# Kernel optimization log

Hardware: AMD Instinct MI355X
Metric: run time of the kernel (lower is better)

## Reference

```python
import jax, jax.numpy as jnp
import numpy as np

H = 2        # attention heads (GENsConv heads=2)
DH = 128     # per-head dim (= hidden_channels; concat=False -> heads averaged)
L = 4        # num message-passing layers actually used (convs[:-1])
NG = 500     # number of graphs in the batch
N = 50000    # total nodes
E = 200000   # total edges
HID = 128    # hidden_channels
RES = 0.1    # initial_res
EPS = 1e-5   # BatchNorm eps (eval mode: running_mean=0, running_var=1)


def _bn(x, g, b):
    # BatchNorm1d in eval mode with default running stats
    return x * (g / jnp.sqrt(1.0 + EPS)) + b


def setup_inputs() -> dict:
    key = jax.random.key(0)
    ks = jax.random.split(key, 32)
    s = 0.05
    d = {}
    d["x"] = jax.random.randint(ks[0], (N,), 0, 30)
    d["edge_index"] = jax.random.randint(ks[1], (2, E), 0, N)
    d["edge_attr"] = jax.random.randint(ks[2], (E,), 0, 30)
    d["batch"] = jnp.sort(jax.random.randint(ks[3], (N,), 0, NG))
    d["node_emb"] = jax.random.normal(ks[4], (30, HID)) * s
    d["emb_w1"] = jax.random.normal(ks[5], (HID, HID)) * s
    d["emb_b1"] = jnp.zeros((HID,))
    d["emb_g1"] = jnp.ones((HID,))
    d["emb_bt1"] = jnp.zeros((HID,))
    d["emb_w2"] = jax.random.normal(ks[6], (HID, HID)) * s
    d["emb_b2"] = jnp.zeros((HID,))
    d["bn0_g"] = jnp.ones((HID,))
    d["bn0_b"] = jnp.zeros((HID,))
    d["Wq"] = jax.random.normal(ks[7], (L, HID, H * DH)) * s
    d["Wk"] = jax.random.normal(ks[8], (L, HID, H * DH)) * s
    d["Wv"] = jax.random.normal(ks[9], (L, HID, H * DH)) * s
    d["We"] = jax.random.normal(ks[10], (L, HID, H * DH)) * s
    d["att"] = jax.random.normal(ks[11], (L, H, DH)) * s
    d["Wroot"] = jax.random.normal(ks[12], (L, HID, HID)) * s
    d["bias"] = jnp.zeros((L, HID))
    d["out_w1"] = jax.random.normal(ks[13], (HID * (L + 1), HID)) * s
    d["out_b1"] = jnp.zeros((HID,))
    d["out_g1"] = jnp.ones((HID,))
    d["out_bt1"] = jnp.zeros((HID,))
    d["out_w2"] = jax.random.normal(ks[14], (HID, 1)) * s
    d["out_b2"] = jnp.zeros((1,))
    return d


def _forward(params, x, edge_index, edge_attr, batch):
    (node_emb, emb_w1, emb_b1, emb_g1, emb_bt1, emb_w2, emb_b2, bn0_g, bn0_b,
     Wq, Wk, Wv, We, att, Wroot, bias,
     out_w1, out_b1, out_g1, out_bt1, out_w2, out_b2) = params
    src, dst = edge_index[0], edge_index[1]
    h = node_emb[x]                      # [N, HID]
    ea = node_emb[edge_attr]             # [E, HID] (original embeds edge_attr with node_embedding)
    # emb_convs: Linear -> BN -> ReLU -> Linear, then bns[0] + ReLU
    h = jax.nn.relu(_bn(h @ emb_w1 + emb_b1, emb_g1, emb_bt1))
    h = h @ emb_w2 + emb_b2
    h = jax.nn.relu(_bn(h, bn0_g, bn0_b))
    x0 = h
    xs = [h]
    for i in range(L):
        hi = xs[-1]
        # gather -> per-edge multi-head attention message -> scatter (GENsConv stand-in)
        q = (hi @ Wq[i]).reshape(N, H, DH)[dst]          # [E, H, DH]
        k = (hi @ Wk[i]).reshape(N, H, DH)[src]
        v = (hi @ Wv[i]).reshape(N, H, DH)[src]
        e = (ea @ We[i]).reshape(E, H, DH)
        score = jnp.einsum('ehd,hd->eh', jax.nn.leaky_relu(q + k + e, 0.2), att[i])
        smax = jax.ops.segment_max(score, dst, num_segments=N)[dst]
        exps = jnp.exp(score - smax)
        denom = jax.ops.segment_sum(exps, dst, num_segments=N)[dst]
        alpha = exps / denom                              # segment softmax over incoming edges
        msg = alpha[..., None] * (v + e)                  # [E, H, DH]
        agg = jax.ops.segment_sum(msg, dst, num_segments=N)  # [N, H, DH]
        out = agg.mean(axis=1) + hi @ Wroot[i] + bias[i]  # concat=False -> average heads, + root
        out = jax.nn.relu(out)
        out = (1.0 - RES) * out + RES * x0                # initial residual
        xs.append(out)
    hc = jnp.concatenate(xs, axis=-1)                     # cat=True -> [N, HID*(L+1)]
    sums = jax.ops.segment_sum(hc, batch, num_segments=NG)
    cnt = jax.ops.segment_sum(jnp.ones((N, 1), hc.dtype), batch, num_segments=NG)
    g = sums / jnp.maximum(cnt, 1.0)                      # global mean pool
    g = jax.nn.relu(_bn(g @ out_w1 + out_b1, out_g1, out_bt1))
    g = g @ out_w2 + out_b2
    return g.reshape(-1)                                  # [NG]


def reference(x, edge_index, edge_attr, batch, node_emb, emb_w1, emb_b1, emb_g1, emb_bt1, emb_w2, emb_b2, bn0_g, bn0_b, Wq, Wk, Wv, We, att, Wroot, bias, out_w1, out_b1, out_g1, out_bt1, out_w2, out_b2):
    params = (node_emb, emb_w1, emb_b1, emb_g1, emb_bt1, emb_w2, emb_b2, bn0_g, bn0_b,
              Wq, Wk, Wv, We, att, Wroot, bias,
              out_w1, out_b1, out_g1, out_bt1, out_w2, out_b2)
    return _forward(params, x, edge_index, edge_attr, batch)
```

## Files before the change

### kernel.cpp

```cpp
#include <hip/hip_runtime.h>
#include <hip/hip_bf16.h>

#define NN 50000
#define NE 200000
#define NGR 500
#define HD 128
#define CDIM 256
#define NLAY 4
#define NVOC 30
#define NCAT 896
#define SCH 256
#define SNB ((NN + SCH - 1) / SCH)
#define GP 7
#define CBP (56 / GP)

static constexpr float BN_INV = 0.9999950000374997f;

typedef __attribute__((ext_vector_type(8))) short bf16x8;
typedef __attribute__((ext_vector_type(4))) float f32x4;
typedef __attribute__((ext_vector_type(2))) float f32x2;

__device__ __forceinline__ float bf2f(unsigned short u) {
    return __uint_as_float(((unsigned)u) << 16);
}
__device__ __forceinline__ unsigned short f2bf(float f) {
    union { __hip_bfloat16 h; unsigned short u; } cv;
    cv.h = __float2bfloat16(f);
    return cv.u;
}
__device__ __forceinline__ f32x2 up2(unsigned u) {
    f32x2 r;
    r.x = __uint_as_float(u << 16);
    r.y = __uint_as_float(u & 0xffff0000u);
    return r;
}
__device__ __forceinline__ f32x2 lk2(f32x2 z) {
    f32x2 zero = {0.f, 0.f};
    return __builtin_elementwise_max(z, zero) + 0.2f * __builtin_elementwise_min(z, zero);
}

__global__ __launch_bounds__(128) void k_tables_node(
    const float* __restrict__ ne, const float* __restrict__ w1, const float* __restrict__ b1,
    const float* __restrict__ g1, const float* __restrict__ bt1,
    const float* __restrict__ w2, const float* __restrict__ b2,
    const float* __restrict__ g0, const float* __restrict__ bt0,
    float* __restrict__ x0tab)
{
    int r = blockIdx.x, d = threadIdx.x;
    __shared__ float emb[HD], t1[HD];
    emb[d] = ne[r * HD + d];
    __syncthreads();
    float acc = b1[d];
    for (int k = 0; k < HD; ++k) acc += emb[k] * w1[k * HD + d];
    float t = fmaxf(acc * BN_INV * g1[d] + bt1[d], 0.f);
    t1[d] = t;
    __syncthreads();
    float acc2 = b2[d];
    for (int k = 0; k < HD; ++k) acc2 += t1[k] * w2[k * HD + d];
    x0tab[r * HD + d] = fmaxf(acc2 * BN_INV * g0[d] + bt0[d], 0.f);
}

__global__ __launch_bounds__(256) void k_tables_edge(
    const float* __restrict__ ne, const float* __restrict__ We, unsigned short* __restrict__ etab)
{
    int la = blockIdx.x;
    int l = la / NVOC, a = la % NVOC;
    int c = threadIdx.x;
    __shared__ float emb[HD];
    if (c < HD) emb[c] = ne[a * HD + c];
    __syncthreads();
    const float* W = We + (size_t)l * HD * CDIM;
    float acc = 0.f;
    for (int k = 0; k < HD; ++k) acc += emb[k] * W[k * CDIM + c];
    etab[(size_t)la * CDIM + c] = f2bf(acc);
}

__global__ __launch_bounds__(64) void k_packw(
    const float* __restrict__ Wq, const float* __restrict__ Wk,
    const float* __restrict__ Wv, const float* __restrict__ Wr,
    unsigned short* __restrict__ Wpk)
{
    int b = blockIdx.x;
    int l = b / 224, rem = b % 224;
    int kb = rem / 56, jb = rem % 56;
    int lane = threadIdx.x;
    int j = jb * 16 + (lane & 15);
    int kbase = kb * 32 + ((lane >> 4) << 3);
    unsigned short* dst = Wpk + ((size_t)b * 64 + lane) * 8;
#pragma unroll
    for (int t = 0; t < 8; ++t) {
        int k = kbase + t;
        float v;
        if (j < 256) {
            v = Wq[((size_t)l * HD + k) * CDIM + j];
        } else if (j < 768) {
            int tt = j - 256, g = tt >> 3, r = tt & 7;
            int c = g * 4 + (r & 3);
            v = (r < 4) ? Wk[((size_t)l * HD + k) * CDIM + c]
                        : Wv[((size_t)l * HD + k) * CDIM + c];
        } else {
            v = Wr[((size_t)l * HD + k) * HD + (j - 768)];
        }
        dst[t] = f2bf(v);
    }
}

__global__ void k_hist_dst(const int* __restrict__ ei, int* __restrict__ cnt)
{
    int e = blockIdx.x * blockDim.x + threadIdx.x;
    if (e < NE) atomicAdd(&cnt[ei[NE + e]], 1);
}

__global__ __launch_bounds__(256) void k_blocksum(const int* __restrict__ cnt, int* __restrict__ part)
{
    int t = threadIdx.x;
    int i = blockIdx.x * SCH + t;
    int v = (i < NN) ? cnt[i] : 0;
    __shared__ int sm[256];
    sm[t] = v;
    __syncthreads();
    for (int off = 128; off; off >>= 1) {
        if (t < off) sm[t] += sm[t + off];
        __syncthreads();
    }
    if (t == 0) part[blockIdx.x] = sm[0];
}

__global__ __launch_bounds__(256) void k_scanpart(int* __restrict__ part)
{
    int t = threadIdx.x;
    int v = (t < SNB) ? part[t] : 0;
    __shared__ int sm[256];
    sm[t] = v;
    __syncthreads();
    for (int off = 1; off < 256; off <<= 1) {
        int u = (t >= off) ? sm[t - off] : 0;
        __syncthreads();
        sm[t] += u;
        __syncthreads();
    }
    if (t < SNB) part[t] = sm[t] - v;
}

__global__ __launch_bounds__(256) void k_csrwrite(
    const int* __restrict__ cnt, const int* __restrict__ part,
    int* __restrict__ rowp, int* __restrict__ wof)
{
    int t = threadIdx.x;
    int i = blockIdx.x * SCH + t;
    int v = (i < NN) ? cnt[i] : 0;
    __shared__ int sm[256];
    sm[t] = v;
    __syncthreads();
    for (int off = 1; off < 256; off <<= 1) {
        int u = (t >= off) ? sm[t - off] : 0;
        __syncthreads();
        sm[t] += u;
        __syncthreads();
    }
    int excl = sm[t] - v + part[blockIdx.x];
    if (i < NN) { rowp[i] = excl; wof[i] = excl; }
    if (i == NN - 1) rowp[NN] = excl + v;
}

__global__ void k_scatter(const int* __restrict__ ei, const int* __restrict__ ea,
                          int* __restrict__ wof, int2* __restrict__ cse)
{
    int e = blockIdx.x * blockDim.x + threadIdx.x;
    if (e < NE) {
        int d = ei[NE + e];
        int pos = atomicAdd(&wof[d], 1);
        int2 v; v.x = ei[e]; v.y = ea[e];
        cse[pos] = v;
    }
}

__global__ void k_x0(const int* __restrict__ x, const float* __restrict__ tab,
                     unsigned short* __restrict__ x0b,
                     const int* __restrict__ batch, int* __restrict__ gptr)
{
    int idx = blockIdx.x * blockDim.x + threadIdx.x;
    if (idx <= NGR) {
        if (idx == NGR) gptr[idx] = NN;
        else {
            int lo = 0, hi = NN;
            while (lo < hi) { int mid = (lo + hi) >> 1; if (batch[mid] < idx) lo = mid + 1; else hi = mid; }
            gptr[idx] = lo;
        }
    }
    if (idx >= NN * 32) return;
    int n = idx >> 5, c = idx & 31;
    float4 v = *(const float4*)&tab[x[n] * HD + c * 4];
    ushort4 u; u.x = f2bf(v.x); u.y = f2bf(v.y); u.z = f2bf(v.z); u.w = f2bf(v.w);
    *(ushort4*)&x0b[(size_t)n * HD + c * 4] = u;
}

__global__ __launch_bounds__(256) void k_gemm(
    const unsigned short* __restrict__ Ab, const unsigned short* __restrict__ Wpk,
    unsigned short* __restrict__ C)
{
    __shared__ unsigned short tile[64][136];
    int lane = threadIdx.x & 63, wid = threadIdx.x >> 6;
    int nb = blockIdx.x * 64;
    int rowl = wid * 16 + (lane & 15);
    int node = nb + rowl;
    size_t arow = (size_t)((node < NN) ? node : (NN - 1));
    int ko = (lane >> 4) << 3;
    const unsigned short* ap = Ab + arow * HD + ko;
    bf16x8 a0 = *(const bf16x8*)(ap);
    bf16x8 a1 = *(const bf16x8*)(ap + 32);
    bf16x8 a2 = *(const bf16x8*)(ap + 64);
    bf16x8 a3 = *(const bf16x8*)(ap + 96);

    int cb0 = blockIdx.y * CBP;
    const unsigned short* bp = Wpk + (size_t)cb0 * 512 + (size_t)lane * 8;
    int jreg = (lane >> 4) << 2;
#pragma unroll 4
    for (int i = 0; i < CBP; ++i) {
        bf16x8 w0 = *(const bf16x8*)(bp + i * 512);
        bf16x8 w1 = *(const bf16x8*)(bp + i * 512 + 28672);
        bf16x8 w2 = *(const bf16x8*)(bp + i * 512 + 57344);
        bf16x8 w3 = *(const bf16x8*)(bp + i * 512 + 86016);
        f32x4 acc = {0.f, 0.f, 0.f, 0.f};
        acc = __builtin_amdgcn_mfma_f32_16x16x32_bf16(w0, a0, acc, 0, 0, 0);
        acc = __builtin_amdgcn_mfma_f32_16x16x32_bf16(w1, a1, acc, 0, 0, 0);
        acc = __builtin_amdgcn_mfma_f32_16x16x32_bf16(w2, a2, acc, 0, 0, 0);
        acc = __builtin_amdgcn_mfma_f32_16x16x32_bf16(w3, a3, acc, 0, 0, 0);
        uint2 o;
        o.x = (unsigned)f2bf(acc[0]) | ((unsigned)f2bf(acc[1]) << 16);
        o.y = (unsigned)f2bf(acc[2]) | ((unsigned)f2bf(acc[3]) << 16);
        *(uint2*)&tile[rowl][i * 16 + jreg] = o;
    }
    __syncthreads();
    int r0 = threadIdx.x >> 4;
    int cseg = (threadIdx.x & 15) * 8;
#pragma unroll
    for (int pass = 0; pass < 4; ++pass) {
        int row = pass * 16 + r0;
        int gnode = nb + row;
        if (gnode < NN) {
            uint4 v = *(const uint4*)&tile[row][cseg];
            *(uint4*)&C[(size_t)gnode * NCAT + cb0 * 16 + cseg] = v;
        }
    }
}

__global__ __launch_bounds__(256) void k_edge(
    const unsigned short* __restrict__ QKVR,
    const unsigned short* __restrict__ etab,
    const float* __restrict__ attL, const float* __restrict__ biasL,
    const unsigned short* __restrict__ x0b,
    const int* __restrict__ rowptr, const int2* __restrict__ cse,
    unsigned short* __restrict__ hb)
{
    int n = (blockIdx.x * blockDim.x + threadIdx.x) >> 6;
    if (n >= NN) return;
    int lane = threadIdx.x & 63;
    int head = lane >> 5, sub = lane & 31;
    int col = head * HD + sub * 4;
    int kvo = 256 + head * 256 + sub * 8;

    uint2 quu = *(const uint2*)&QKVR[(size_t)n * NCAT + col];
    f32x2 q0 = up2(quu.x), q1 = up2(quu.y);
    float4 a4 = *(const float4*)&attL[col];
    f32x2 av0 = {a4.x, a4.y}, av1 = {a4.z, a4.w};

    float l0 = 0.f, l1 = 0.f;
    f32x2 accA0 = {0.f, 0.f}, accA1 = {0.f, 0.f};
    f32x2 accB0 = {0.f, 0.f}, accB1 = {0.f, 0.f};

    int beg = rowptr[n], end = rowptr[n + 1];
    int idx = beg;
    for (; idx + 1 < end; idx += 2) {
        int2 seA = cse[idx];
        int2 seB = cse[idx + 1];
        uint4 kvA = *(const uint4*)&QKVR[(size_t)seA.x * NCAT + kvo];
        uint4 kvB = *(const uint4*)&QKVR[(size_t)seB.x * NCAT + kvo];
        uint2 euA = *(const uint2*)&etab[seA.y * CDIM + col];
        uint2 euB = *(const uint2*)&etab[seB.y * CDIM + col];

        f32x2 eA0 = up2(euA.x), eA1 = up2(euA.y);
        f32x2 eB0 = up2(euB.x), eB1 = up2(euB.y);

        f32x2 zA0 = lk2(q0 + up2(kvA.x) + eA0);
        f32x2 zA1 = lk2(q1 + up2(kvA.y) + eA1);
        f32x2 zB0 = lk2(q0 + up2(kvB.x) + eB0);
        f32x2 zB1 = lk2(q1 + up2(kvB.y) + eB1);

        f32x2 ppA = zA0 * av0 + zA1 * av1;
        f32x2 ppB = zB0 * av0 + zB1 * av1;
        float pA = ppA.x + ppA.y;
        float pB = ppB.x + ppB.y;
        pA += __shfl_xor(pA, 16); pB += __shfl_xor(pB, 16);
        pA += __shfl_xor(pA, 8);  pB += __shfl_xor(pB, 8);
        pA += __shfl_xor(pA, 4);  pB += __shfl_xor(pB, 4);
        pA += __shfl_xor(pA, 2);  pB += __shfl_xor(pB, 2);
        pA += __shfl_xor(pA, 1);  pB += __shfl_xor(pB, 1);
        float peA = __expf(fminf(fmaxf(pA, -30.f), 30.f));
        float peB = __expf(fminf(fmaxf(pB, -30.f), 30.f));

        accA0 += peA * (up2(kvA.z) + eA0);
        accA1 += peA * (up2(kvA.w) + eA1);
        accB0 += peB * (up2(kvB.z) + eB0);
        accB1 += peB * (up2(kvB.w) + eB1);
        l0 += peA;
        l1 += peB;
    }
    if (idx < end) {
        int2 se = cse[idx];
        uint4 kv = *(const uint4*)&QKVR[(size_t)se.x * NCAT + kvo];
        uint2 eu = *(const uint2*)&etab[se.y * CDIM + col];
        f32x2 e0 = up2(eu.x), e1 = up2(eu.y);
        f32x2 z0 = lk2(q0 + up2(kv.x) + e0);
        f32x2 z1 = lk2(q1 + up2(kv.y) + e1);
        f32x2 pp = z0 * av0 + z1 * av1;
        float p = pp.x + pp.y;
        p += __shfl_xor(p, 16); p += __shfl_xor(p, 8);
        p += __shfl_xor(p, 4);  p += __shfl_xor(p, 2); p += __shfl_xor(p, 1);
        float pe = __expf(fminf(fmaxf(p, -30.f), 30.f));
        accA0 += pe * (up2(kv.z) + e0);
        accA1 += pe * (up2(kv.w) + e1);
        l0 += pe;
    }
    float l = l0 + l1;
    float invl = (l > 0.f) ? 1.0f / l : 0.f;
    f32x2 r0 = (accA0 + accB0) * invl;
    f32x2 r1 = (accA1 + accB1) * invl;
    r0.x = 0.5f * (r0.x + __shfl_xor(r0.x, 32));
    r0.y = 0.5f * (r0.y + __shfl_xor(r0.y, 32));
    r1.x = 0.5f * (r1.x + __shfl_xor(r1.x, 32));
    r1.y = 0.5f * (r1.y + __shfl_xor(r1.y, 32));
    if (head == 0) {
        uint2 ruu = *(const uint2*)&QKVR[(size_t)n * NCAT + 768 + sub * 4];
        f32x2 ru0 = up2(ruu.x), ru1 = up2(ruu.y);
        float4 b4 = *(const float4*)&biasL[sub * 4];
        f32x2 bb0 = {b4.x, b4.y}, bb1 = {b4.z, b4.w};
        uint2 xuu = *(const uint2*)&x0b[(size_t)n * HD + sub * 4];
        f32x2 xx0 = up2(xuu.x), xx1 = up2(xuu.y);
        f32x2 zero = {0.f, 0.f};
        f32x2 h0 = 0.9f * __builtin_elementwise_max(r0 + ru0 + bb0, zero) + 0.1f * xx0;
        f32x2 h1 = 0.9f * __builtin_elementwise_max(r1 + ru1 + bb1, zero) + 0.1f * xx1;
        ushort4 o;
        o.x = f2bf(h0.x); o.y = f2bf(h0.y); o.z = f2bf(h1.x); o.w = f2bf(h1.y);
        *(ushort4*)&hb[(size_t)n * HD + sub * 4] = o;
    }
}

__global__ __launch_bounds__(256) void k_poolall(
    const unsigned short* __restrict__ x0b,
    const unsigned short* __restrict__ h0, const unsigned short* __restrict__ h1,
    const unsigned short* __restrict__ h2, const unsigned short* __restrict__ h3,
    const int* __restrict__ gptr, float* __restrict__ gsum)
{
    int g = blockIdx.x, sl = blockIdx.y;
    const unsigned short* src = (sl == 0) ? x0b : (sl == 1) ? h0 : (sl == 2) ? h1
                              : (sl == 3) ? h2 : h3;
    int q = threadIdx.x & 31;
    int r = threadIdx.x >> 5;
    int beg = gptr[g], end = gptr[g + 1];
    float sx = 0.f, sy = 0.f, sz = 0.f, sw = 0.f;
    for (int n = beg + r; n < end; n += 8) {
        uint2 u = *(const uint2*)&src[(size_t)n * HD + q * 4];
        sx += __uint_as_float(u.x << 16);
        sy += __uint_as_float(u.x & 0xffff0000u);
        sz += __uint_as_float(u.y << 16);
        sw += __uint_as_float(u.y & 0xffff0000u);
    }
    __shared__ float4 sm[8][32];
    float4 s4 = {sx, sy, sz, sw};
    sm[r][q] = s4;
    __syncthreads();
    if (r == 0) {
        float4 t = sm[0][q];
#pragma unroll
        for (int j = 1; j < 8; ++j) {
            float4 u = sm[j][q];
            t.x += u.x; t.y += u.y; t.z += u.z; t.w += u.w;
        }
        *(float4*)&gsum[(size_t)g * 640 + sl * HD + q * 4] = t;
    }
}

__global__ __launch_bounds__(128) void k_out(
    const float* __restrict__ gsum, const int* __restrict__ gptr,
    const float* __restrict__ w1, const float* __restrict__ b1,
    const float* __restrict__ g1, const float* __restrict__ bt1,
    const float* __restrict__ w2, const float* __restrict__ b2,
    float* __restrict__ out)
{
    int g = blockIdx.x, d = threadIdx.x;
    __shared__ float row[640];
    __shared__ float red[2];
    int c = gptr[g + 1] - gptr[g];
    float invc = 1.0f / (float)max(c, 1);
    for (int j = d; j < 640; j += 128) row[j] = gsum[(size_t)g * 640 + j] * invc;
    __syncthreads();
    float acc = b1[d];
    for (int j = 0; j < 640; ++j) acc += row[j] * w1[j * HD + d];
    float val = fmaxf(acc * BN_INV * g1[d] + bt1[d], 0.f);
    float part = val * w2[d];
    part += __shfl_xor(part, 32); part += __shfl_xor(part, 16);
    part += __shfl_xor(part, 8);  part += __shfl_xor(part, 4);
    part += __shfl_xor(part, 2);  part += __shfl_xor(part, 1);
    if ((threadIdx.x & 63) == 0) red[threadIdx.x >> 6] = part;
    __syncthreads();
    if (threadIdx.x == 0) out[g] = red[0] + red[1] + b2[0];
}

extern "C" void kernel_launch(void* const* d_in, const int* in_sizes, int n_in,
                              void* d_out, int out_size, void* d_ws, size_t ws_size,
                              hipStream_t stream)
{
    const int*   x        = (const int*)d_in[0];
    const int*   ei       = (const int*)d_in[1];
    const int*   ea       = (const int*)d_in[2];
    const int*   batch    = (const int*)d_in[3];
    const float* node_emb = (const float*)d_in[4];
    const float* emb_w1   = (const float*)d_in[5];
    const float* emb_b1   = (const float*)d_in[6];
    const float* emb_g1   = (const float*)d_in[7];
    const float* emb_bt1  = (const float*)d_in[8];
    const float* emb_w2   = (const float*)d_in[9];
    const float* emb_b2   = (const float*)d_in[10];
    const float* bn0_g    = (const float*)d_in[11];
    const float* bn0_b    = (const float*)d_in[12];
    const float* Wq       = (const float*)d_in[13];
    const float* Wk       = (const float*)d_in[14];
    const float* Wv       = (const float*)d_in[15];
    const float* We       = (const float*)d_in[16];
    const float* att      = (const float*)d_in[17];
    const float* Wroot    = (const float*)d_in[18];
    const float* bias     = (const float*)d_in[19];
    const float* out_w1   = (const float*)d_in[20];
    const float* out_b1   = (const float*)d_in[21];
    const float* out_g1   = (const float*)d_in[22];
    const float* out_bt1  = (const float*)d_in[23];
    const float* out_w2   = (const float*)d_in[24];
    const float* out_b2   = (const float*)d_in[25];

    char* wp = (char*)d_ws;
    auto alloc = [&](size_t bytes) -> void* {
        void* p = (void*)wp;
        wp += (bytes + 255) & ~(size_t)255;
        return p;
    };
    unsigned short* x0b   = (unsigned short*)alloc((size_t)NN * HD * 2);
    unsigned short* hb0   = (unsigned short*)alloc((size_t)NN * HD * 2);
    unsigned short* hb1   = (unsigned short*)alloc((size_t)NN * HD * 2);
    unsigned short* hb2   = (unsigned short*)alloc((size_t)NN * HD * 2);
    unsigned short* hb3   = (unsigned short*)alloc((size_t)NN * HD * 2);
    unsigned short* QKVR  = (unsigned short*)alloc((size_t)NN * NCAT * 2);
    float*          x0tab = (float*)alloc((size_t)NVOC * HD * 4);
    unsigned short* etab  = (unsigned short*)alloc((size_t)NLAY * NVOC * CDIM * 2);
    unsigned short* Wpk   = (unsigned short*)alloc((size_t)NLAY * 224 * 64 * 8 * 2);
    int*   cnt   = (int*)alloc((size_t)NN * 4);
    int*   rowp  = (int*)alloc((size_t)(NN + 1) * 4);
    int*   wof   = (int*)alloc((size_t)(NN + 1) * 4);
    int*   part  = (int*)alloc((size_t)SNB * 4);
    int2*  cse   = (int2*)alloc((size_t)NE * 8);
    int*   gptr  = (int*)alloc((size_t)(NGR + 1) * 4);
    float* gsum  = (float*)alloc((size_t)NGR * 640 * 4);

    hipMemsetAsync(cnt, 0, (size_t)NN * 4, stream);

    k_tables_node<<<NVOC, 128, 0, stream>>>(node_emb, emb_w1, emb_b1, emb_g1, emb_bt1,
                                            emb_w2, emb_b2, bn0_g, bn0_b, x0tab);
    k_tables_edge<<<NLAY * NVOC, 256, 0, stream>>>(node_emb, We, etab);
    k_packw<<<NLAY * 224, 64, 0, stream>>>(Wq, Wk, Wv, Wroot, Wpk);
    k_hist_dst<<<(NE + 255) / 256, 256, 0, stream>>>(ei, cnt);
    k_blocksum<<<SNB, 256, 0, stream>>>(cnt, part);
    k_scanpart<<<1, 256, 0, stream>>>(part);
    k_csrwrite<<<SNB, 256, 0, stream>>>(cnt, part, rowp, wof);
    k_scatter<<<(NE + 255) / 256, 256, 0, stream>>>(ei, ea, wof, cse);
    k_x0<<<(NN * 32 + 255) / 256, 256, 0, stream>>>(x, x0tab, x0b, batch, gptr);

    const unsigned short* hin = x0b;
    unsigned short* houts[NLAY] = {hb0, hb1, hb2, hb3};
    for (int l = 0; l < NLAY; ++l) {
        k_gemm<<<dim3((NN + 63) / 64, GP), 256, 0, stream>>>(
            hin, Wpk + (size_t)l * 224 * 512, QKVR);
        k_edge<<<(NN * 64 + 255) / 256, 256, 0, stream>>>(
            QKVR, etab + (size_t)l * NVOC * CDIM, att + (size_t)l * CDIM, bias + (size_t)l * HD,
            x0b, rowp, cse, houts[l]);
        hin = houts[l];
    }
    k_poolall<<<dim3(NGR, 5), 256, 0, stream>>>(x0b, hb0, hb1, hb2, hb3, gptr, gsum);
    k_out<<<NGR, 128, 0, stream>>>(gsum, gptr, out_w1, out_b1, out_g1, out_bt1,
                                   out_w2, out_b2, (float*)d_out);
}
```

Measured before the change: 409.3 us.

## Merge setup kernels into one launch and software-pipeline edge gathers

Four independent setup kernels (node table, edge table, weight packing, destination histogram) are combined into a single launch that dispatches on block index, removing three launch gaps. Separately, the edge aggregation loop now prefetches the next pair of neighbor K/V and edge-table rows before computing on the current pair, to hide gather latency. The prefetch raises register pressure in the edge kernel, which may lower occupancy.

```diff
diff --git a/kernel.cpp b/kernel.cpp
--- a/kernel.cpp
+++ b/kernel.cpp
@@ -14,6 +14,12 @@
 #define GP 7
 #define CBP (56 / GP)
 
+#define SU_TBLN 30
+#define SU_TBLE (NLAY * NVOC)
+#define SU_PKW  (NLAY * 224 / 4)
+#define SU_HIST ((NE + 255) / 256)
+#define SU_NBLK (SU_TBLN + SU_TBLE + SU_PKW + SU_HIST)
+
 static constexpr float BN_INV = 0.9999950000374997f;
 
 typedef __attribute__((ext_vector_type(8))) short bf16x8;
@@ -39,76 +45,77 @@
     return __builtin_elementwise_max(z, zero) + 0.2f * __builtin_elementwise_min(z, zero);
 }
 
-__global__ __launch_bounds__(128) void k_tables_node(
-    const float* __restrict__ ne, const float* __restrict__ w1, const float* __restrict__ b1,
+__global__ __launch_bounds__(256) void k_setup(
+    const float* __restrict__ ne,
+    const float* __restrict__ w1, const float* __restrict__ b1,
     const float* __restrict__ g1, const float* __restrict__ bt1,
     const float* __restrict__ w2, const float* __restrict__ b2,
     const float* __restrict__ g0, const float* __restrict__ bt0,
-    float* __restrict__ x0tab)
-{
-    int r = blockIdx.x, d = threadIdx.x;
-    __shared__ float emb[HD], t1[HD];
-    emb[d] = ne[r * HD + d];
-    __syncthreads();
-    float acc = b1[d];
-    for (int k = 0; k < HD; ++k) acc += emb[k] * w1[k * HD + d];
-    float t = fmaxf(acc * BN_INV * g1[d] + bt1[d], 0.f);
-    t1[d] = t;
-    __syncthreads();
-    float acc2 = b2[d];
-    for (int k = 0; k < HD; ++k) acc2 += t1[k] * w2[k * HD + d];
-    x0tab[r * HD + d] = fmaxf(acc2 * BN_INV * g0[d] + bt0[d], 0.f);
-}
-
-__global__ __launch_bounds__(256) void k_tables_edge(
-    const float* __restrict__ ne, const float* __restrict__ We, unsigned short* __restrict__ etab)
-{
-    int la = blockIdx.x;
-    int l = la / NVOC, a = la % NVOC;
-    int c = threadIdx.x;
-    __shared__ float emb[HD];
-    if (c < HD) emb[c] = ne[a * HD + c];
-    __syncthreads();
-    const float* W = We + (size_t)l * HD * CDIM;
-    float acc = 0.f;
-    for (int k = 0; k < HD; ++k) acc += emb[k] * W[k * CDIM + c];
-    etab[(size_t)la * CDIM + c] = f2bf(acc);
-}
-
-__global__ __launch_bounds__(64) void k_packw(
+    const float* __restrict__ We,
     const float* __restrict__ Wq, const float* __restrict__ Wk,
     const float* __restrict__ Wv, const float* __restrict__ Wr,
-    unsigned short* __restrict__ Wpk)
-{
-    int b = blockIdx.x;
-    int l = b / 224, rem = b % 224;
-    int kb = rem / 56, jb = rem % 56;
-    int lane = threadIdx.x;
-    int j = jb * 16 + (lane & 15);
-    int kbase = kb * 32 + ((lane >> 4) << 3);
-    unsigned short* dst = Wpk + ((size_t)b * 64 + lane) * 8;
+    const int* __restrict__ ei,
+    float* __restrict__ x0tab, unsigned short* __restrict__ etab,
+    unsigned short* __restrict__ Wpk, int* __restrict__ cnt)
+{
+    __shared__ float smem[256];
+    int b = blockIdx.x, t = threadIdx.x;
+    if (b < SU_TBLN) {
+        int r = b, d = t;
+        if (d < HD) smem[d] = ne[r * HD + d];
+        __syncthreads();
+        float v1 = 0.f;
+        if (d < HD) {
+            float acc = b1[d];
+            for (int k = 0; k < HD; ++k) acc += smem[k] * w1[k * HD + d];
+            v1 = fmaxf(acc * BN_INV * g1[d] + bt1[d], 0.f);
+        }
+        __syncthreads();
+        if (d < HD) smem[HD + d] = v1;
+        __syncthreads();
+        if (d < HD) {
+            float acc2 = b2[d];
+            for (int k = 0; k < HD; ++k) acc2 += smem[HD + k] * w2[k * HD + d];
+            x0tab[r * HD + d] = fmaxf(acc2 * BN_INV * g0[d] + bt0[d], 0.f);
+        }
+    } else if (b < SU_TBLN + SU_TBLE) {
+        int la = b - SU_TBLN;
+        int l = la / NVOC, a = la % NVOC;
+        int c = t;
+        if (c < HD) smem[c] = ne[a * HD + c];
+        __syncthreads();
+        const float* W = We + (size_t)l * HD * CDIM;
+        float acc = 0.f;
+        for (int k = 0; k < HD; ++k) acc += smem[k] * W[k * CDIM + c];
+        etab[(size_t)la * CDIM + c] = f2bf(acc);
+    } else if (b < SU_TBLN + SU_TBLE + SU_PKW) {
+        int bb = (b - SU_TBLN - SU_TBLE) * 4 + (t >> 6);
+        int lane = t & 63;
+        int l = bb / 224, rem = bb % 224;
+        int kb = rem / 56, jb = rem % 56;
+        int j = jb * 16 + (lane & 15);
+        int kbase = kb * 32 + ((lane >> 4) << 3);
+        unsigned short* dst = Wpk + ((size_t)bb * 64 + lane) * 8;
 #pragma unroll
-    for (int t = 0; t < 8; ++t) {
-        int k = kbase + t;
-        float v;
-        if (j < 256) {
-            v = Wq[((size_t)l * HD + k) * CDIM + j];
-        } else if (j < 768) {
-            int tt = j - 256, g = tt >> 3, r = tt & 7;
-            int c = g * 4 + (r & 3);
-            v = (r < 4) ? Wk[((size_t)l * HD + k) * CDIM + c]
-                        : Wv[((size_t)l * HD + k) * CDIM + c];
-        } else {
-            v = Wr[((size_t)l * HD + k) * HD + (j - 768)];
-        }
-        dst[t] = f2bf(v);
-    }
-}
-
-__global__ void k_hist_dst(const int* __restrict__ ei, int* __restrict__ cnt)
-{
-    int e = blockIdx.x * blockDim.x + threadIdx.x;
-    if (e < NE) atomicAdd(&cnt[ei[NE + e]], 1);
+        for (int tt = 0; tt < 8; ++tt) {
+            int k = kbase + tt;
+            float v;
+            if (j < 256) {
+                v = Wq[((size_t)l * HD + k) * CDIM + j];
+            } else if (j < 768) {
+                int t2 = j - 256, g = t2 >> 3, r = t2 & 7;
+                int c = g * 4 + (r & 3);
+                v = (r < 4) ? Wk[((size_t)l * HD + k) * CDIM + c]
+                            : Wv[((size_t)l * HD + k) * CDIM + c];
+            } else {
+                v = Wr[((size_t)l * HD + k) * HD + (j - 768)];
+            }
+            dst[tt] = f2bf(v);
+        }
+    } else {
+        int e = (b - SU_TBLN - SU_TBLE - SU_PKW) * 256 + t;
+        if (e < NE) atomicAdd(&cnt[ei[NE + e]], 1);
+    }
 }
 
 __global__ __launch_bounds__(256) void k_blocksum(const int* __restrict__ cnt, int* __restrict__ part)
@@ -271,14 +278,27 @@
 
     int beg = rowptr[n], end = rowptr[n + 1];
     int idx = beg;
-    for (; idx + 1 < end; idx += 2) {
-        int2 seA = cse[idx];
-        int2 seB = cse[idx + 1];
-        uint4 kvA = *(const uint4*)&QKVR[(size_t)seA.x * NCAT + kvo];
-        uint4 kvB = *(const uint4*)&QKVR[(size_t)seB.x * NCAT + kvo];
-        uint2 euA = *(const uint2*)&etab[seA.y * CDIM + col];
-        uint2 euB = *(const uint2*)&etab[seB.y * CDIM + col];
-
+    uint4 kvA, kvB;
+    uint2 euA, euB;
+    bool have = (idx + 1 < end);
+    if (have) {
+        int2 sA = cse[idx], sB = cse[idx + 1];
+        kvA = *(const uint4*)&QKVR[(size_t)sA.x * NCAT + kvo];
+        kvB = *(const uint4*)&QKVR[(size_t)sB.x * NCAT + kvo];
+        euA = *(const uint2*)&etab[sA.y * CDIM + col];
+        euB = *(const uint2*)&etab[sB.y * CDIM + col];
+    }
+    while (have) {
+        bool nhave = (idx + 3 < end);
+        uint4 nkvA, nkvB;
+        uint2 neuA, neuB;
+        if (nhave) {
+            int2 sA = cse[idx + 2], sB = cse[idx + 3];
+            nkvA = *(const uint4*)&QKVR[(size_t)sA.x * NCAT + kvo];
+            nkvB = *(const uint4*)&QKVR[(size_t)sB.x * NCAT + kvo];
+            neuA = *(const uint2*)&etab[sA.y * CDIM + col];
+            neuB = *(const uint2*)&etab[sB.y * CDIM + col];
+        }
         f32x2 eA0 = up2(euA.x), eA1 = up2(euA.y);
         f32x2 eB0 = up2(euB.x), eB1 = up2(euB.y);
 
@@ -305,6 +325,10 @@
         accB1 += peB * (up2(kvB.w) + eB1);
         l0 += peA;
         l1 += peB;
+
+        kvA = nkvA; kvB = nkvB; euA = neuA; euB = neuB;
+        idx += 2;
+        have = nhave;
     }
     if (idx < end) {
         int2 se = cse[idx];
@@ -463,11 +487,9 @@
 
     hipMemsetAsync(cnt, 0, (size_t)NN * 4, stream);
 
-    k_tables_node<<<NVOC, 128, 0, stream>>>(node_emb, emb_w1, emb_b1, emb_g1, emb_bt1,
-                                            emb_w2, emb_b2, bn0_g, bn0_b, x0tab);
-    k_tables_edge<<<NLAY * NVOC, 256, 0, stream>>>(node_emb, We, etab);
-    k_packw<<<NLAY * 224, 64, 0, stream>>>(Wq, Wk, Wv, Wroot, Wpk);
-    k_hist_dst<<<(NE + 255) / 256, 256, 0, stream>>>(ei, cnt);
+    k_setup<<<SU_NBLK, 256, 0, stream>>>(
+        node_emb, emb_w1, emb_b1, emb_g1, emb_bt1, emb_w2, emb_b2, bn0_g, bn0_b,
+        We, Wq, Wk, Wv, Wroot, ei, x0tab, etab, Wpk, cnt);
     k_blocksum<<<SNB, 256, 0, stream>>>(cnt, part);
     k_scanpart<<<1, 256, 0, stream>>>(part);
     k_csrwrite<<<SNB, 256, 0, stream>>>(cnt, part, rowp, wof);
```

Result: no change. 412.7 us (+0.8%).
